# Kernel optimization log

Measured on AMD Instinct MI355X. Metric: run time of the kernel, lower is better.

Reference implementation:

```python
import jax, jax.numpy as jnp
import numpy as np

NEG_INF = float('-inf')
B, T, C, U = 32, 1000, 500, 100
RISK_FACTOR = 0.1  # risk_strategy='exp', group_strategy='end'


def _lse3(x1, x2, x3):
    # numerically-safe logsumexp of 3 args, nan-free grads at -inf
    m = jnp.maximum(jnp.maximum(x1, x2), x3)
    dead = jnp.isneginf(m)
    ms = jnp.where(dead, 0.0, m)
    s = jnp.exp(x1 - ms) + jnp.exp(x2 - ms) + jnp.exp(x3 - ms)
    s = jnp.where(dead, 1.0, s)
    return jnp.where(dead, NEG_INF, ms + jnp.log(s))


def _safe_lse(x, axis):
    m = jnp.max(x, axis=axis, keepdims=True)
    dead = jnp.isneginf(m)
    ms = jnp.where(dead, 0.0, m)
    s = jnp.sum(jnp.exp(x - ms), axis=axis, keepdims=True)
    s = jnp.where(dead, 1.0, s)
    out = jnp.where(dead, NEG_INF, ms + jnp.log(s))
    return jnp.squeeze(out, axis)


def _log_sub_exp(a, b):
    # faithful port of espnet's log_substraction_exp: log(exp(a)-exp(b))
    mask1 = (~jnp.isinf(a)) & (~jnp.isinf(b))
    a_ = jnp.where(mask1, a, -1.0)
    b_ = jnp.where(mask1, b, -2.0)
    ans_tmp = b_ + jnp.log(jnp.exp(a_ - b_) - 1.0)
    a2 = jnp.where(jnp.isinf(ans_tmp), -2000.0, a_)
    b2 = jnp.where(jnp.isinf(ans_tmp), -2001.0, b_)
    ans1 = b2 + jnp.log(jnp.exp(a2 - b2) - 1.0)
    ans = jnp.where(mask1, ans1, jnp.full_like(a, NEG_INF))
    mask2 = (~jnp.isinf(a)) & jnp.isinf(b)
    return jnp.where(mask2, a, ans)


def _shift_r(x, n):
    return jnp.pad(x[:, :-n], ((0, 0), (n, 0)), constant_values=NEG_INF)


def _shift_l(x, n):
    return jnp.pad(x[:, n:], ((0, 0), (0, n)), constant_values=NEG_INF)


def _brctc_loss(nnet_output, ys_pad, hlens, ylens):
    # Dense equivalent of the k2 CTC lattice forward-backward in the log semiring.
    Bb, Tt, Cc = nnet_output.shape
    Uu = ys_pad.shape[1]
    S = 2 * Uu + 1  # extended label states: blank,y1,blank,...,yU,blank
    dt = nnet_output.dtype
    s_idx = jnp.arange(S)
    lab = ys_pad[:, jnp.clip((s_idx - 1) // 2, 0, Uu - 1)]        # [B,S]
    labels_ext = jnp.where((s_idx % 2 == 1)[None, :], lab, 0)
    prev_lab = ys_pad[:, jnp.clip((s_idx - 3) // 2, 0, Uu - 1)]
    allow_skip = ((s_idx % 2 == 1) & (s_idx >= 3))[None, :] & (lab != prev_lab)
    # p_ext[b,t,s] = nnet_output[b,t,labels_ext[b,s]]
    p_ext = jnp.take_along_axis(
        nnet_output, jnp.broadcast_to(labels_ext[:, None, :], (Bb, Tt, S)), axis=2)
    valid_s = s_idx[None, :] <= 2 * ylens[:, None]                # states beyond 2*ylen don't exist
    p_ext = jnp.where(valid_s[:, None, :], p_ext, NEG_INF)
    p_tbs = jnp.transpose(p_ext, (1, 0, 2))                       # [T,B,S]

    # forward: alpha[t,s] includes emission at frame t
    def fstep(a, pt):
        anew = pt + _lse3(a, _shift_r(a, 1),
                          jnp.where(allow_skip, _shift_r(a, 2), NEG_INF))
        return anew, anew
    a0 = jnp.full((Bb, S), NEG_INF, dt).at[:, 0].set(0.0)  # virtual start state
    _, alpha = jax.lax.scan(fstep, a0, p_tbs)                     # [T,B,S]

    # backward: beta[t,s] covers frames t+1..hlen-1 (excludes emission at t)
    t_arr = jnp.arange(Tt)
    fin = (s_idx[None, :] == 2 * ylens[:, None]) | (s_idx[None, :] == 2 * ylens[:, None] - 1)
    beta_fin = jnp.where(fin, 0.0, NEG_INF).astype(dt)
    allow_skip_n2 = jnp.pad(allow_skip[:, 2:], ((0, 0), (0, 2)), constant_values=False)
    p_next = jnp.concatenate([p_tbs[1:], jnp.full((1, Bb, S), NEG_INF, dt)], axis=0)

    def bstep(bcarry, inp):
        t, pn = inp
        q = pn + bcarry
        cand = _lse3(q, _shift_l(q, 1),
                     jnp.where(allow_skip_n2, _shift_l(q, 2), NEG_INF))
        bnew = jnp.where((t == hlens - 1)[:, None], beta_fin, cand)
        return bnew, bnew
    _, beta = jax.lax.scan(bstep, jnp.full((Bb, S), NEG_INF, dt),
                           (t_arr, p_next), reverse=True)         # [T,B,S]

    alpha = jnp.transpose(alpha, (1, 2, 0))                       # [B,S,T]
    beta = jnp.transpose(beta, (1, 2, 0))
    alpha = jnp.where((t_arr[None, :] < hlens[:, None])[:, None, :], alpha, NEG_INF)

    # keep only label (odd) states, as in alpha[:, 1::2]
    a_l = alpha[:, 1::2, :]
    b_l = beta[:, 1::2, :]
    p_l = jnp.transpose(p_ext, (0, 2, 1))[:, 1::2, :]
    dead = jnp.isneginf(a_l)  # states absent from the lattice
    b_l = jnp.where(dead, NEG_INF, b_l)
    p_l = jnp.where(dead, NEG_INF, p_l)

    # beta' removes the self-loop continuation -> posterior of label u ending at t
    beta_prime = _log_sub_exp(b_l[:, :, :-1], b_l[:, :, 1:] + p_l[:, :, 1:])
    beta_prime = jnp.concatenate([beta_prime, b_l[:, :, -1:]], axis=-1)
    loss_state = a_l + beta_prime                                 # [B,U,T]

    # risk_strategy == 'exp': risk = -risk_factor * t / hlen
    risk = -RISK_FACTOR * (t_arr[None, None, :].astype(dt) / hlens[:, None, None].astype(dt))
    loss_state = loss_state + risk

    loss_u = _safe_lse(loss_state, 2)                             # [B,U]
    mask = ~jnp.isneginf(loss_u)
    last = jnp.sum(mask.astype(jnp.int32), axis=1) - 1            # = ylen-1
    loss = jnp.take_along_axis(loss_u, last[:, None], axis=1)[:, 0]
    return -loss


def setup_inputs():
    key = jax.random.key(0)
    k1, k2, k3, k4 = jax.random.split(key, 4)
    nnet_output = jax.nn.log_softmax(
        jax.random.normal(k1, (B, T, C), dtype=jnp.float32), axis=-1)
    ys_pad = jax.random.randint(k2, (B, U), 1, C, dtype=jnp.int32)  # labels, 0 = blank excluded
    ylens = jax.random.randint(k3, (B,), 80, U + 1, dtype=jnp.int32)
    hlens = jax.random.randint(k4, (B,), 800, T + 1, dtype=jnp.int32)
    return {'nnet_output': nnet_output, 'ys_pad': ys_pad, 'hlens': hlens, 'ylens': ylens}


def reference(nnet_output, ys_pad, hlens, ylens):
    return _brctc_loss(nnet_output, ys_pad, hlens, ylens)
```

## Files before the change

kernel.cpp:

```cpp
#include <hip/hip_runtime.h>
#include <math.h>

#define T_DIM 1000
#define C_DIM 500
#define U_DIM 100
#define PAD   16
#define AROWS (T_DIM + 5)
#define NEGINF (-INFINITY)
#define LROW  128

typedef float v2f __attribute__((ext_vector_type(2)));

__device__ __forceinline__ v2f splat2(float x) { v2f r; r[0] = x; r[1] = x; return r; }

__device__ __forceinline__ v2f lse2p(v2f X, v2f Y) {
    v2f m, mn;
    m[0]  = fmaxf(X[0], Y[0]); m[1]  = fmaxf(X[1], Y[1]);
    mn[0] = fminf(X[0], Y[0]); mn[1] = fminf(X[1], Y[1]);
    v2f d = mn - m;
    v2f e; e[0] = __expf(d[0]); e[1] = __expf(d[1]);
    v2f s = splat2(1.0f) + e;
    v2f l; l[0] = __logf(s[0]); l[1] = __logf(s[1]);
    v2f r = m + l;
    r[0] = (m[0] == NEGINF) ? NEGINF : r[0];
    r[1] = (m[1] == NEGINF) ? NEGINF : r[1];
    return r;
}

__device__ __forceinline__ v2f lse3p(v2f x1, v2f x2, v2f x3) {
    v2f m;
    m[0] = fmaxf(fmaxf(x1[0], x2[0]), x3[0]);
    m[1] = fmaxf(fmaxf(x1[1], x2[1]), x3[1]);
    v2f d1 = x1 - m, d2 = x2 - m, d3 = x3 - m;
    v2f e1, e2, e3;
    e1[0] = __expf(d1[0]); e1[1] = __expf(d1[1]);
    e2[0] = __expf(d2[0]); e2[1] = __expf(d2[1]);
    e3[0] = __expf(d3[0]); e3[1] = __expf(d3[1]);
    v2f s = (e1 + e2) + e3;
    v2f l; l[0] = __logf(s[0]); l[1] = __logf(s[1]);
    v2f r = m + l;
    r[0] = (m[0] == NEGINF) ? NEGINF : r[0];
    r[1] = (m[1] == NEGINF) ? NEGINF : r[1];
    return r;
}

__device__ __forceinline__ float lse3f(float x1, float x2, float x3) {
    float m = fmaxf(fmaxf(x1, x2), x3);
    if (m == NEGINF) return NEGINF;
    return m + __logf(__expf(x1 - m) + __expf(x2 - m) + __expf(x3 - m));
}

__device__ __forceinline__ float log_sub_expf(float a, float b) {
    bool ia = isinf(a), ib = isinf(b);
    if (!ia && !ib) {
        float ans = b + __logf(__expf(a - b) - 1.0f);
        if (isinf(ans)) ans = -2001.0f + __logf(__expf(1.0f) - 1.0f);
        return ans;
    }
    if (!ia && ib) return a;
    return NEGINF;
}

__device__ __forceinline__ float dpp_shr1(float x) {
    int r = __builtin_amdgcn_update_dpp(__float_as_int(NEGINF), __float_as_int(x),
                                        0x138, 0xF, 0xF, false);
    return __int_as_float(r);
}
__device__ __forceinline__ float dpp_shl1(float x) {
    int r = __builtin_amdgcn_update_dpp(__float_as_int(NEGINF), __float_as_int(x),
                                        0x130, 0xF, 0xF, false);
    return __int_as_float(r);
}

#define FWD_STEP(tt, PL, PBV)                                                \
    {                                                                        \
        v2f P02 = mz02 + splat2(PBV);                                        \
        float am1 = dpp_shr1(A13[1]);                                        \
        v2f Y;  Y[0] = am1;  Y[1] = A13[0];                                  \
        v2f x3; x3[0] = skip1 ? am1 : NEGINF;                                \
        x3[1] = skip3 ? A13[0] : NEGINF;                                     \
        v2f n02 = P02 + lse2p(A02, Y);                                       \
        v2f n13 = (PL) + lse3p(A13, A02, x3);                                \
        A02 = n02; A13 = n13;                                                \
        if (st)                                                              \
            ((float2*)(Ab + (size_t)(tt) * U_DIM))[L] =                      \
                make_float2(n13[0], n13[1]);                                 \
    }

#define BWD_STEP(tt, PL, PBV)                                                \
    {                                                                        \
        v2f Q02 = (mz02 + splat2(PBV)) + B02;                                \
        v2f Q13 = (PL) + B13;                                                \
        float qd0 = dpp_shl1(Q02[0]);                                        \
        float qd1 = dpp_shl1(Q13[0]);                                        \
        v2f x2; x2[0] = Q02[1]; x2[1] = qd0;                                 \
        v2f x3; x3[0] = skipA ? Q13[1] : NEGINF;                             \
        x3[1] = skipB ? qd1 : NEGINF;                                        \
        v2f n02 = lse2p(Q02, Q13);                                           \
        v2f n13 = lse3p(Q13, x2, x3);                                        \
        bool fin = ((tt) == hl - 1);                                         \
        B02[0] = fin ? f0 : n02[0]; B02[1] = fin ? f2 : n02[1];              \
        B13[0] = fin ? f1 : n13[0]; B13[1] = fin ? f3 : n13[1];              \
        if (st)                                                              \
            ((float2*)(Bb + (size_t)(tt) * U_DIM))[L] =                      \
                make_float2(B13[0], B13[1]);                                 \
    }

#define LDF(buf, rr) (((const v2f*)((buf) + (rr) * LROW))[L])

#define LSTEP(tt, RA, RB, RP)                                                \
    {                                                                        \
        float a_nx = (RA), br_nx = (RB), p_nx = (RP);                        \
        float bl   = (a_t  == NEGINF) ? NEGINF : braw_t;                     \
        float term = (a_nx == NEGINF) ? NEGINF : (br_nx + p_nx);             \
        float bp = log_sub_expf(bl, term);                                   \
        float x = a_t + bp - 0.1f * (float)(tt) * inv_hl;                    \
        if (x != NEGINF) {                                                   \
            float nm = fmaxf(m, x);                                          \
            ssum = ssum * __expf(m - nm) + __expf(x - nm);                   \
            m = nm;                                                          \
        }                                                                    \
        a_t = a_nx; braw_t = br_nx;                                          \
    }

__device__ __forceinline__ void gather_chunk(
    const float* __restrict__ nb, const int* __restrict__ shY, int yl,
    float* __restrict__ lds, float* __restrict__ ldsb,
    float* __restrict__ Pg ,
    int row0, int j)
{
#pragma unroll
    for (int k = 0; k < 15; ++k) {
        int i = j + k * 448;
        if (i < 6400) {
            int r = i >> 7, q = i & 127;
            if (q <= 100) {
                int row = row0 + r;
                int col = (q < 100) ? shY[q] : 0;
                float v = (row < T_DIM) ? nb[(size_t)row * C_DIM + col] : NEGINF;
                if (q < 100) {
                    lds[r * LROW + q] = (q < yl) ? v : NEGINF;
                    if (Pg) Pg[(size_t)r * U_DIM + q] = v;
                } else {
                    ldsb[r] = v;
                }
            }
        }
    }
}

extern "C" __global__ void __launch_bounds__(1024)
brctc_fused(const float* __restrict__ nnet, const int* __restrict__ ys,
            const int* __restrict__ hlens, const int* __restrict__ ylens,
            float* __restrict__ P,
            float* __restrict__ A, float* __restrict__ Braw,
            float* __restrict__ out)
{
    const int b = blockIdx.x;
    const int tid = threadIdx.x;
    const int w = tid >> 6, L = tid & 63;
    const int hl = hlens[b], yl = ylens[b];
    const size_t TP = T_DIM + 2 * PAD;
    const float* nb = nnet + (size_t)b * T_DIM * C_DIM;
    float* Pw = P + ((size_t)b * TP + PAD) * U_DIM;
    const float* Pb = Pw;
    const int* ysb = ys + b * U_DIM;
    float* Ab = A    + (size_t)b * AROWS * U_DIM;
    float* Bb = Braw + (size_t)b * AROWS * U_DIM;

    __shared__ __align__(16) float fbuf[2][50 * LROW];
    __shared__ __align__(16) float bbuf[2][50 * LROW];
    __shared__ float fpb[2][56], bpb[2][56];
    __shared__ float shm[8][U_DIM], shs[8][U_DIM], shlu[U_DIM];
    __shared__ int shY[U_DIM];

    if (tid < U_DIM) shY[tid] = ysb[tid];

    const int s0_ = 4 * L, s1 = 4 * L + 1, s2_ = 4 * L + 2, s3 = 4 * L + 3;
    const int u1 = 2 * L;
    const int lab1 = ysb[min(u1, U_DIM - 1)];
    const int lab3 = ysb[min(u1 + 1, U_DIM - 1)];
    const int labm = ysb[min(max(u1 - 1, 0), U_DIM - 1)];
    const int labn = ysb[min(u1 + 2, U_DIM - 1)];
    const bool skip1 = (s1 >= 3) && (lab1 != labm);
    const bool skip3 = (lab3 != lab1);
    const bool skipA = (s1 < 199) && (lab3 != lab1);
    const bool skipB = (s3 < 199) && (labn != lab3);
    const int ty = 2 * yl;
    const bool v0 = (s0_ <= 200) && (s0_ <= ty);
    const bool v2_ = (s2_ <= 200) && (s2_ <= ty);
    const bool st = (L < 50);
    v2f mz02; mz02[0] = v0 ? 0.0f : NEGINF; mz02[1] = v2_ ? 0.0f : NEGINF;
    const float f0 = (s0_ == ty || s0_ == ty - 1) ? 0.0f : NEGINF;
    const float f1 = (s1  == ty || s1  == ty - 1) ? 0.0f : NEGINF;
    const float f2 = (s2_ == ty || s2_ == ty - 1) ? 0.0f : NEGINF;
    const float f3 = (s3  == ty || s3  == ty - 1) ? 0.0f : NEGINF;

    v2f A02, A13, B02, B13;
    A02[0] = (L == 0) ? 0.0f : NEGINF; A02[1] = NEGINF;
    A13[0] = NEGINF; A13[1] = NEGINF;
    B02[0] = NEGINF; B02[1] = NEGINF;
    B13[0] = NEGINF; B13[1] = NEGINF;

    __syncthreads();

    if (w >= 2) {
        int j2 = tid - 128;
        for (int i = j2; i < 4 * 50 * 28; i += 896) {
            int buf = i / (50 * 28), rem = i % (50 * 28);
            int r = rem / 28, q = 100 + rem % 28;
            float* base = (buf == 0) ? fbuf[0] : (buf == 1) ? fbuf[1]
                        : (buf == 2) ? bbuf[0] : bbuf[1];
            base[r * LROW + q] = NEGINF;
        }
    }
    if (w >= 2 && w < 9) {
        int j = tid - 128;
        gather_chunk(nb, shY, yl, fbuf[0], fpb[0], Pw, 0, j);
        if (j < U_DIM) Pw[(size_t)T_DIM * U_DIM + j] = NEGINF;
    } else if (w >= 9) {
        int j = tid - 576;
        gather_chunk(nb, shY, yl, bbuf[0], bpb[0], nullptr, 951, j);
    }
    __syncthreads();

    for (int c = 0; c < 20; ++c) {
        if (w == 0) {
            const float* fb = fbuf[c & 1];
            const float* fp = fpb[c & 1];
            const int tb = 50 * c;
            for (int kk = 0; kk < 50; kk += 10) {
                v2f r0 = LDF(fb, kk + 0), r1 = LDF(fb, kk + 1);
                v2f r2 = LDF(fb, kk + 2), r3 = LDF(fb, kk + 3);
                v2f r4 = LDF(fb, kk + 4), r5 = LDF(fb, kk + 5);
                v2f r6 = LDF(fb, kk + 6), r7 = LDF(fb, kk + 7);
                v2f r8 = LDF(fb, kk + 8), r9 = LDF(fb, kk + 9);
                float g0 = fp[kk + 0], g1 = fp[kk + 1], g2 = fp[kk + 2];
                float g3 = fp[kk + 3], g4 = fp[kk + 4], g5 = fp[kk + 5];
                float g6 = fp[kk + 6], g7 = fp[kk + 7], g8 = fp[kk + 8];
                float g9 = fp[kk + 9];
                FWD_STEP(tb + kk + 0, r0, g0)
                FWD_STEP(tb + kk + 1, r1, g1)
                FWD_STEP(tb + kk + 2, r2, g2)
                FWD_STEP(tb + kk + 3, r3, g3)
                FWD_STEP(tb + kk + 4, r4, g4)
                FWD_STEP(tb + kk + 5, r5, g5)
                FWD_STEP(tb + kk + 6, r6, g6)
                FWD_STEP(tb + kk + 7, r7, g7)
                FWD_STEP(tb + kk + 8, r8, g8)
                FWD_STEP(tb + kk + 9, r9, g9)
            }
        } else if (w == 1) {
            const float* bbf = bbuf[c & 1];
            const float* bp  = bpb[c & 1];
            const int cc = 19 - c;
            const int tb = 50 * cc;
            for (int kk = 49; kk >= 9; kk -= 10) {
                v2f r0 = LDF(bbf, kk - 0), r1 = LDF(bbf, kk - 1);
                v2f r2 = LDF(bbf, kk - 2), r3 = LDF(bbf, kk - 3);
                v2f r4 = LDF(bbf, kk - 4), r5 = LDF(bbf, kk - 5);
                v2f r6 = LDF(bbf, kk - 6), r7 = LDF(bbf, kk - 7);
                v2f r8 = LDF(bbf, kk - 8), r9 = LDF(bbf, kk - 9);
                float g0 = bp[kk - 0], g1 = bp[kk - 1], g2 = bp[kk - 2];
                float g3 = bp[kk - 3], g4 = bp[kk - 4], g5 = bp[kk - 5];
                float g6 = bp[kk - 6], g7 = bp[kk - 7], g8 = bp[kk - 8];
                float g9 = bp[kk - 9];
                BWD_STEP(tb + kk - 0, r0, g0)
                BWD_STEP(tb + kk - 1, r1, g1)
                BWD_STEP(tb + kk - 2, r2, g2)
                BWD_STEP(tb + kk - 3, r3, g3)
                BWD_STEP(tb + kk - 4, r4, g4)
                BWD_STEP(tb + kk - 5, r5, g5)
                BWD_STEP(tb + kk - 6, r6, g6)
                BWD_STEP(tb + kk - 7, r7, g7)
                BWD_STEP(tb + kk - 8, r8, g8)
                BWD_STEP(tb + kk - 9, r9, g9)
            }
        } else if (c < 19) {
            if (w < 9) {
                int j = tid - 128;
                int row0 = (c + 1) * 50;
                gather_chunk(nb, shY, yl, fbuf[(c + 1) & 1], fpb[(c + 1) & 1],
                             Pw + (size_t)row0 * U_DIM, row0, j);
            } else {
                int j = tid - 576;
                int row0 = (18 - c) * 50 + 1;
                gather_chunk(nb, shY, yl, bbuf[(c + 1) & 1], bpb[(c + 1) & 1],
                             nullptr, row0, j);
            }
        }
        __syncthreads();
    }

    {
        const int r0f = min(hl, T_DIM);
        const int nrow = T_DIM + 1 - r0f;
        const int tot = nrow * 50;
        for (int i = tid; i < tot; i += 1024) {
            const int rr = r0f + i / 50, cc2 = i % 50;
            ((float2*)(Ab + (size_t)rr * U_DIM))[cc2] = make_float2(NEGINF, NEGINF);
        }
    }
    __syncthreads();

    {
        const int u = tid & 127;
        const int c = tid >> 7;
        if (u < U_DIM) {
            const bool valu = (u < yl);
            const float inv_hl = 1.0f / (float)hl;
            const int t0 = 125 * c;
            float a_t    = Ab[(size_t)t0 * U_DIM + u];
            float braw_t = Bb[(size_t)t0 * U_DIM + u];
            float aA0 = Ab[(long)(t0 + 1) * U_DIM + u];
            float aA1 = Ab[(long)(t0 + 2) * U_DIM + u];
            float aA2 = Ab[(long)(t0 + 3) * U_DIM + u];
            float aA3 = Ab[(long)(t0 + 4) * U_DIM + u];
            float bA0 = Bb[(long)(t0 + 1) * U_DIM + u];
            float bA1 = Bb[(long)(t0 + 2) * U_DIM + u];
            float bA2 = Bb[(long)(t0 + 3) * U_DIM + u];
            float bA3 = Bb[(long)(t0 + 4) * U_DIM + u];
            float pA0 = valu ? Pb[(long)(t0 + 1) * U_DIM + u] : NEGINF;
            float pA1 = valu ? Pb[(long)(t0 + 2) * U_DIM + u] : NEGINF;
            float pA2 = valu ? Pb[(long)(t0 + 3) * U_DIM + u] : NEGINF;
            float pA3 = valu ? Pb[(long)(t0 + 4) * U_DIM + u] : NEGINF;
            float m = NEGINF, ssum = 0.0f;
            for (int kb = 0; kb <= 120; kb += 4) {
                long nr = (long)(t0 + kb + 5);
                float aB0 = Ab[(nr + 0) * U_DIM + u];
                float aB1 = Ab[(nr + 1) * U_DIM + u];
                float aB2 = Ab[(nr + 2) * U_DIM + u];
                float aB3 = Ab[(nr + 3) * U_DIM + u];
                float bB0 = Bb[(nr + 0) * U_DIM + u];
                float bB1 = Bb[(nr + 1) * U_DIM + u];
                float bB2 = Bb[(nr + 2) * U_DIM + u];
                float bB3 = Bb[(nr + 3) * U_DIM + u];
                float pB0 = valu ? Pb[(nr + 0) * U_DIM + u] : NEGINF;
                float pB1 = valu ? Pb[(nr + 1) * U_DIM + u] : NEGINF;
                float pB2 = valu ? Pb[(nr + 2) * U_DIM + u] : NEGINF;
                float pB3 = valu ? Pb[(nr + 3) * U_DIM + u] : NEGINF;
                LSTEP(t0 + kb + 0, aA0, bA0, pA0)
                LSTEP(t0 + kb + 1, aA1, bA1, pA1)
                LSTEP(t0 + kb + 2, aA2, bA2, pA2)
                LSTEP(t0 + kb + 3, aA3, bA3, pA3)
                aA0 = aB0; aA1 = aB1; aA2 = aB2; aA3 = aB3;
                bA0 = bB0; bA1 = bB1; bA2 = bB2; bA3 = bB3;
                pA0 = pB0; pA1 = pB1; pA2 = pB2; pA3 = pB3;
            }
            LSTEP(t0 + 124, aA0, bA0, pA0)
            shm[c][u] = m; shs[c][u] = ssum;
        }
    }
    __syncthreads();
    if (tid < U_DIM) {
        float M = NEGINF;
#pragma unroll
        for (int c = 0; c < 8; ++c) M = fmaxf(M, shm[c][tid]);
        float lu = NEGINF;
        if (M != NEGINF) {
            float s = 0.0f;
#pragma unroll
            for (int c = 0; c < 8; ++c) {
                float mc = shm[c][tid];
                if (mc != NEGINF) s += shs[c][tid] * __expf(mc - M);
            }
            lu = M + __logf(s);
        }
        shlu[tid] = lu;
    }
    __syncthreads();
    if (tid == 0) {
        int cnt = 0;
        for (int u = 0; u < U_DIM; ++u) cnt += (shlu[u] != NEGINF) ? 1 : 0;
        int last = cnt - 1;
        last = last < 0 ? 0 : (last > U_DIM - 1 ? U_DIM - 1 : last);
        out[b] = -shlu[last];
    }
}

extern "C" __global__ void __launch_bounds__(256)
brctc_fwd_fb(const float* __restrict__ nnet, const int* __restrict__ ys,
             const int* __restrict__ hlens, const int* __restrict__ ylens,
             float* __restrict__ a_l)
{
    const int b = blockIdx.x;
    const int s = threadIdx.x;
    __shared__ float sh_a[201];
    __shared__ int   sh_ys[U_DIM];
    if (s < U_DIM) sh_ys[s] = ys[b * U_DIM + s];
    __syncthreads();
    const int hl = hlens[b], yl = ylens[b];
    int lab = 0; bool skip = false;
    if (s < 201) {
        if (s & 1) lab = sh_ys[(s - 1) >> 1];
        if ((s & 1) && s >= 3) skip = (sh_ys[(s - 1) >> 1] != sh_ys[(s - 3) >> 1]);
        sh_a[s] = (s == 0) ? 0.0f : NEGINF;
    }
    const bool valid = (s < 201) && (s <= 2 * yl);
    const bool isodd = (s < 201) && (s & 1);
    const int l = (s - 1) >> 1;
    const float* base = nnet + (size_t)b * T_DIM * C_DIM;
    float* alb = a_l + (size_t)b * T_DIM * U_DIM;
    __syncthreads();
    float p_cur = valid ? base[lab] : NEGINF;
    for (int t = 0; t < T_DIM; ++t) {
        float p_nxt = (valid && (t + 1 < T_DIM)) ? base[(size_t)(t + 1) * C_DIM + lab] : NEGINF;
        float x1 = (s < 201) ? sh_a[s] : NEGINF;
        float x2 = (s >= 1 && s < 201) ? sh_a[s - 1] : NEGINF;
        float x3 = skip ? sh_a[s - 2] : NEGINF;
        float anew = p_cur + lse3f(x1, x2, x3);
        __syncthreads();
        if (s < 201) sh_a[s] = anew;
        if (isodd) alb[t * U_DIM + l] = (t < hl) ? anew : NEGINF;
        __syncthreads();
        p_cur = p_nxt;
    }
}

extern "C" __global__ void __launch_bounds__(256)
brctc_bwd_fb(const float* __restrict__ nnet, const int* __restrict__ ys,
             const int* __restrict__ hlens, const int* __restrict__ ylens,
             const float* __restrict__ a_l, float* __restrict__ out)
{
    const int b = blockIdx.x;
    const int s = threadIdx.x;
    __shared__ float sh_b[201], sh_q[201], sh_lu[U_DIM];
    __shared__ int sh_ys[U_DIM];
    if (s < U_DIM) sh_ys[s] = ys[b * U_DIM + s];
    __syncthreads();
    const int hl = hlens[b], yl = ylens[b];
    int lab = 0; bool skip2 = false;
    if (s < 201) {
        if (s & 1) lab = sh_ys[(s - 1) >> 1];
        int s2 = s + 2;
        if (s2 < 201 && (s2 & 1) && s2 >= 3)
            skip2 = (sh_ys[(s2 - 1) >> 1] != sh_ys[(s2 - 3) >> 1]);
        sh_b[s] = NEGINF;
    }
    const bool valid = (s < 201) && (s <= 2 * yl);
    const bool isodd = (s < 201) && (s & 1);
    const int l = (s - 1) >> 1;
    const float fin0 = (s == 2 * yl || s == 2 * yl - 1) ? 0.0f : NEGINF;
    const float* base = nnet + (size_t)b * T_DIM * C_DIM;
    const float* alb = a_l + (size_t)b * T_DIM * U_DIM;
    float m_run = NEGINF, acc = 0.0f, prev_bl = NEGINF, p_hi = NEGINF;
    __syncthreads();
    for (int t = T_DIM - 1; t >= 0; --t) {
        float p_lo = valid ? base[(size_t)t * C_DIM + lab] : NEGINF;
        float a_cur = isodd ? alb[t * U_DIM + l] : NEGINF;
        float q = (s < 201) ? (p_hi + sh_b[s]) : NEGINF;
        if (s < 201) sh_q[s] = q;
        __syncthreads();
        float q2 = (s + 1 < 201) ? sh_q[s + 1] : NEGINF;
        float q3 = skip2 ? sh_q[s + 2] : NEGINF;
        float cand = lse3f(q, q2, q3);
        float bnew = (t == hl - 1) ? fin0 : cand;
        if (s < 201) sh_b[s] = bnew;
        if (isodd) {
            float bl_t = (a_cur == NEGINF) ? NEGINF : bnew;
            float bp = (t == T_DIM - 1) ? bl_t : log_sub_expf(bl_t, prev_bl + p_hi);
            float x = a_cur + bp - 0.1f * ((float)t / (float)hl);
            if (x != NEGINF) {
                if (x <= m_run) acc += __expf(x - m_run);
                else { acc = acc * __expf(m_run - x) + 1.0f; m_run = x; }
            }
            prev_bl = bl_t;
        }
        __syncthreads();
        p_hi = p_lo;
    }
    if (isodd) sh_lu[l] = (m_run == NEGINF) ? NEGINF : (m_run + __logf(acc));
    __syncthreads();
    if (s == 0) {
        int cnt = 0;
        for (int u = 0; u < U_DIM; ++u) cnt += (sh_lu[u] != NEGINF) ? 1 : 0;
        int last = cnt - 1;
        last = last < 0 ? 0 : (last > U_DIM - 1 ? U_DIM - 1 : last);
        out[b] = -sh_lu[last];
    }
}

extern "C" void kernel_launch(void* const* d_in, const int* in_sizes, int n_in,
                              void* d_out, int out_size, void* d_ws, size_t ws_size,
                              hipStream_t stream) {
    const float* nnet  = (const float*)d_in[0];
    const int*   ys    = (const int*)d_in[1];
    const int*   hlens = (const int*)d_in[2];
    const int*   ylens = (const int*)d_in[3];
    float*       outp  = (float*)d_out;
    const int B = in_sizes[2];
    const size_t TP = T_DIM + 2 * PAD;
    const size_t szP  = (size_t)B * TP * U_DIM;
    const size_t szA  = (size_t)B * AROWS * U_DIM;
    const size_t need = (szP + 2 * szA) * sizeof(float);

    if (ws_size >= need) {
        float* P    = (float*)d_ws;
        float* A    = P + szP;
        float* Braw = A + szA;
        brctc_fused<<<B, 1024, 0, stream>>>(nnet, ys, hlens, ylens, P, A, Braw, outp);
    } else {
        float* A = (float*)d_ws;
        brctc_fwd_fb<<<B, 256, 0, stream>>>(nnet, ys, hlens, ylens, A);
        brctc_bwd_fb<<<B, 256, 0, stream>>>(nnet, ys, hlens, ylens, A, outp);
    }
}
```

Baseline: 431.8 us.

## Split forward and backward CTC recursions across two wavefronts with LDS relay handoff

The forward and backward recursions each move from a single wavefront handling two state pairs per lane to two wavefronts, each owning half of the label range with one state per lane. Boundary values pass between the wavefronts each step through small LDS relay slots that hold a canary value, with spin-waits and periodic progress counters so the producer does not run too far ahead. The aim is to halve the serial dependency chain per wavefront. In exchange it adds spin-wait latency and LDS round trips on every step, and the gather now runs on fewer wavefronts, each with more iterations.

```diff
diff --git a/kernel.cpp b/kernel.cpp
--- a/kernel.cpp
+++ b/kernel.cpp
@@ -8,42 +8,19 @@
 #define AROWS (T_DIM + 5)
 #define NEGINF (-INFINITY)
 #define LROW  128
-
-typedef float v2f __attribute__((ext_vector_type(2)));
-
-__device__ __forceinline__ v2f splat2(float x) { v2f r; r[0] = x; r[1] = x; return r; }
-
-__device__ __forceinline__ v2f lse2p(v2f X, v2f Y) {
-    v2f m, mn;
-    m[0]  = fmaxf(X[0], Y[0]); m[1]  = fmaxf(X[1], Y[1]);
-    mn[0] = fminf(X[0], Y[0]); mn[1] = fminf(X[1], Y[1]);
-    v2f d = mn - m;
-    v2f e; e[0] = __expf(d[0]); e[1] = __expf(d[1]);
-    v2f s = splat2(1.0f) + e;
-    v2f l; l[0] = __logf(s[0]); l[1] = __logf(s[1]);
-    v2f r = m + l;
-    r[0] = (m[0] == NEGINF) ? NEGINF : r[0];
-    r[1] = (m[1] == NEGINF) ? NEGINF : r[1];
-    return r;
-}
-
-__device__ __forceinline__ v2f lse3p(v2f x1, v2f x2, v2f x3) {
-    v2f m;
-    m[0] = fmaxf(fmaxf(x1[0], x2[0]), x3[0]);
-    m[1] = fmaxf(fmaxf(x1[1], x2[1]), x3[1]);
-    v2f d1 = x1 - m, d2 = x2 - m, d3 = x3 - m;
-    v2f e1, e2, e3;
-    e1[0] = __expf(d1[0]); e1[1] = __expf(d1[1]);
-    e2[0] = __expf(d2[0]); e2[1] = __expf(d2[1]);
-    e3[0] = __expf(d3[0]); e3[1] = __expf(d3[1]);
-    v2f s = (e1 + e2) + e3;
-    v2f l; l[0] = __logf(s[0]); l[1] = __logf(s[1]);
-    v2f r = m + l;
-    r[0] = (m[0] == NEGINF) ? NEGINF : r[0];
-    r[1] = (m[1] == NEGINF) ? NEGINF : r[1];
-    return r;
-}
-
+#define CANU  0x7fbadbadu
+#define CANF  __uint_as_float(CANU)
+
+__device__ __forceinline__ float lse2s(float a, float b) {
+    float m = fmaxf(a, b), mn = fminf(a, b);
+    float r = m + __logf(1.0f + __expf(mn - m));
+    return fmaxf(r, NEGINF);
+}
+__device__ __forceinline__ float lse3s(float x1, float x2, float x3) {
+    float m = fmaxf(fmaxf(x1, x2), x3);
+    float r = m + __logf(__expf(x1 - m) + __expf(x2 - m) + __expf(x3 - m));
+    return fmaxf(r, NEGINF);
+}
 __device__ __forceinline__ float lse3f(float x1, float x2, float x3) {
     float m = fmaxf(fmaxf(x1, x2), x3);
     if (m == NEGINF) return NEGINF;
@@ -71,42 +48,6 @@
                                         0x130, 0xF, 0xF, false);
     return __int_as_float(r);
 }
-
-#define FWD_STEP(tt, PL, PBV)                                                \
-    {                                                                        \
-        v2f P02 = mz02 + splat2(PBV);                                        \
-        float am1 = dpp_shr1(A13[1]);                                        \
-        v2f Y;  Y[0] = am1;  Y[1] = A13[0];                                  \
-        v2f x3; x3[0] = skip1 ? am1 : NEGINF;                                \
-        x3[1] = skip3 ? A13[0] : NEGINF;                                     \
-        v2f n02 = P02 + lse2p(A02, Y);                                       \
-        v2f n13 = (PL) + lse3p(A13, A02, x3);                                \
-        A02 = n02; A13 = n13;                                                \
-        if (st)                                                              \
-            ((float2*)(Ab + (size_t)(tt) * U_DIM))[L] =                      \
-                make_float2(n13[0], n13[1]);                                 \
-    }
-
-#define BWD_STEP(tt, PL, PBV)                                                \
-    {                                                                        \
-        v2f Q02 = (mz02 + splat2(PBV)) + B02;                                \
-        v2f Q13 = (PL) + B13;                                                \
-        float qd0 = dpp_shl1(Q02[0]);                                        \
-        float qd1 = dpp_shl1(Q13[0]);                                        \
-        v2f x2; x2[0] = Q02[1]; x2[1] = qd0;                                 \
-        v2f x3; x3[0] = skipA ? Q13[1] : NEGINF;                             \
-        x3[1] = skipB ? qd1 : NEGINF;                                        \
-        v2f n02 = lse2p(Q02, Q13);                                           \
-        v2f n13 = lse3p(Q13, x2, x3);                                        \
-        bool fin = ((tt) == hl - 1);                                         \
-        B02[0] = fin ? f0 : n02[0]; B02[1] = fin ? f2 : n02[1];              \
-        B13[0] = fin ? f1 : n13[0]; B13[1] = fin ? f3 : n13[1];              \
-        if (st)                                                              \
-            ((float2*)(Bb + (size_t)(tt) * U_DIM))[L] =                      \
-                make_float2(B13[0], B13[1]);                                 \
-    }
-
-#define LDF(buf, rr) (((const v2f*)((buf) + (rr) * LROW))[L])
 
 #define LSTEP(tt, RA, RB, RP)                                                \
     {                                                                        \
@@ -130,8 +71,8 @@
     int row0, int j)
 {
 #pragma unroll
-    for (int k = 0; k < 15; ++k) {
-        int i = j + k * 448;
+    for (int k = 0; k < 17; ++k) {
+        int i = j + k * 384;
         if (i < 6400) {
             int r = i >> 7, q = i & 127;
             if (q <= 100) {
@@ -149,6 +90,143 @@
     }
 }
 
+#define FWP(j, pOv, gv)                                                      \
+    {                                                                        \
+        const int t_ = tbk + (j);                                            \
+        float Osh = dpp_shr1(O0);                                            \
+        float nE = (mzE_lo + (gv)) + lse2s(E0, Osh);                         \
+        float nO = (pOv) + lse3s(O0, E0, Osh + mskFlo);                      \
+        float nOsh = dpp_shr1(nO);                                           \
+        volatile float* rp = (L == 50)                                       \
+            ? (volatile float*)(rlyF + 2 * (t_ & 31)) : dmp;                 \
+        rp[0] = nOsh; rp[1] = nE;               \
+        E0 = nE; O0 = nO;                                                    \
+        if (st) stA[(j) * U_DIM] = nO;                                       \
+    }
+
+#define FWC(j, pOv, gv)                                                      \
+    {                                                                        \
+        const int t_ = tbk + (j);                                            \
+        const int sl_ = (t_ + 31) & 31;                                      \
+        float r0 = *(volatile const float*)(rlyF + 2 * sl_);                 \
+        float r1 = *(volatile const float*)(rlyF + 2 * sl_ + 1);             \
+        while (__float_as_uint(r0) == CANU || __float_as_uint(r1) == CANU) { \
+            __builtin_amdgcn_s_sleep(1);                                     \
+            r0 = *(volatile const float*)(rlyF + 2 * sl_);                   \
+            r1 = *(volatile const float*)(rlyF + 2 * sl_ + 1);               \
+        }                                                                    \
+        asm volatile("" ::: "memory");                                       \
+        float Esh = dpp_shr1(E0); Esh = (L == 0) ? r1 : Esh;                 \
+        float Osh = dpp_shr1(O0); Osh = (L == 0) ? r0 : Osh;                 \
+        float nE = (mzE_hi + (gv)) + lse2s(E0, O0);                          \
+        float nO = (pOv) + lse3s(O0, Esh, Osh + mskFhi);                     \
+        volatile float* cp = (L == 0)                                        \
+            ? (volatile float*)(rlyF + 2 * sl_) : dmp;                       \
+        cp[0] = CANF; cp[1] = CANF;                                          \
+        E0 = nE; O0 = nO;                                                    \
+        if (st) stA[(j) * U_DIM] = nO;                                       \
+        if (((t_) & 7) == 7) {                                               \
+            asm volatile("s_waitcnt lgkmcnt(0)" ::: "memory");               \
+            volatile int* pp = (L == 0) ? (volatile int*)&prgFC              \
+                                        : (volatile int*)dmp;                \
+            *pp = t_ + 1;                                                    \
+        }                                                                    \
+    }
+
+#define BWP(j, pOv, gv, FINF)                                                \
+    {                                                                        \
+        const int t_ = tbk - (j);                                            \
+        const int k_ = 999 - t_;                                             \
+        float qE = (mzE_hi + (gv)) + BE;                                     \
+        float qO = (pOv) + BO;                                               \
+        volatile float* rp = (L == 0)                                        \
+            ? (volatile float*)(rlyB + (k_ & 31)) : dmp;                     \
+        rp[0] = qO;                                                          \
+        float qOsh = dpp_shl1(qO);                                           \
+        float nE = lse2s(qE, qOsh);                                          \
+        float nO = lse3s(qO, qE, qOsh + mskBhi);                             \
+        if (FINF) { const bool fin = (t_ == hl1);                            \
+            BE = fin ? fE_hi : nE; BO = fin ? fO_hi : nO;                    \
+        } else { BE = nE; BO = nO; }                                         \
+        if (st) stB[-(int)((j) * U_DIM)] = BO;                               \
+    }
+
+#define BWC(j, pOv, gv, FINF)                                                \
+    {                                                                        \
+        const int t_ = tbk - (j);                                            \
+        const int k_ = 999 - t_;                                             \
+        const int sl_ = k_ & 31;                                             \
+        float r0 = *(volatile const float*)(rlyB + sl_);                     \
+        while (__float_as_uint(r0) == CANU) {                                \
+            __builtin_amdgcn_s_sleep(1);                                     \
+            r0 = *(volatile const float*)(rlyB + sl_);                       \
+        }                                                                    \
+        asm volatile("" ::: "memory");                                       \
+        float qE = (mzE_lo + (gv)) + BE;                                     \
+        float qO = (pOv) + BO;                                               \
+        qO = (L == 50) ? r0 : qO;                                            \
+        float qEsh = dpp_shl1(qE);                                           \
+        float qOsh = dpp_shl1(qO);                                           \
+        float nE = lse2s(qE, qO);                                            \
+        float nO = lse3s(qO, qEsh, qOsh + mskBlo);                           \
+        volatile float* cp = (L == 0)                                        \
+            ? (volatile float*)(rlyB + sl_) : dmp;                           \
+        cp[0] = CANF;                                                        \
+        if (FINF) { const bool fin = (t_ == hl1);                            \
+            BE = fin ? fE_lo : nE; BO = fin ? fO_lo : nO;                    \
+        } else { BE = nE; BO = nO; }                                         \
+        if (st) stB[-(int)((j) * U_DIM)] = BO;                               \
+        if ((k_ & 7) == 7) {                                                 \
+            asm volatile("s_waitcnt lgkmcnt(0)" ::: "memory");               \
+            volatile int* pp = (L == 0) ? (volatile int*)&prgBC              \
+                                        : (volatile int*)dmp;                \
+            *pp = k_ + 1;                                                    \
+        }                                                                    \
+    }
+
+#define BWP_BLOCK(FINF)                                                      \
+    {                                                                        \
+        const int kst = 999 - (tb2 + kk);                                    \
+        if (kst >= 30) {                                                     \
+            const int need = kst - 21;                                       \
+            while (*(volatile int*)&prgBC < need)                            \
+                __builtin_amdgcn_s_sleep(8);                                 \
+            asm volatile("" ::: "memory");                                   \
+        }                                                                    \
+        const int tbk = tb2 + kk;                                            \
+        float p0 = bb2[(kk-0)*LROW + 50 + L], p1 = bb2[(kk-1)*LROW + 50 + L],\
+              p2 = bb2[(kk-2)*LROW + 50 + L], p3 = bb2[(kk-3)*LROW + 50 + L],\
+              p4 = bb2[(kk-4)*LROW + 50 + L], p5 = bb2[(kk-5)*LROW + 50 + L],\
+              p6 = bb2[(kk-6)*LROW + 50 + L], p7 = bb2[(kk-7)*LROW + 50 + L],\
+              p8 = bb2[(kk-8)*LROW + 50 + L], p9 = bb2[(kk-9)*LROW + 50 + L];\
+        float g0 = bp2[kk-0], g1 = bp2[kk-1], g2 = bp2[kk-2], g3 = bp2[kk-3],\
+              g4 = bp2[kk-4], g5 = bp2[kk-5], g6 = bp2[kk-6], g7 = bp2[kk-7],\
+              g8 = bp2[kk-8], g9 = bp2[kk-9];                                \
+        BWP(0,p0,g0,FINF) BWP(1,p1,g1,FINF) BWP(2,p2,g2,FINF)                \
+        BWP(3,p3,g3,FINF) BWP(4,p4,g4,FINF) BWP(5,p5,g5,FINF)                \
+        BWP(6,p6,g6,FINF) BWP(7,p7,g7,FINF) BWP(8,p8,g8,FINF)                \
+        BWP(9,p9,g9,FINF)                                                    \
+        stB -= 10 * U_DIM;                                                   \
+    }
+
+#define BWC_BLOCK(FINF)                                                      \
+    {                                                                        \
+        const int tbk = tb2 + kk;                                            \
+        float p0 = bb2[(kk-0)*LROW + L], p1 = bb2[(kk-1)*LROW + L],          \
+              p2 = bb2[(kk-2)*LROW + L], p3 = bb2[(kk-3)*LROW + L],          \
+              p4 = bb2[(kk-4)*LROW + L], p5 = bb2[(kk-5)*LROW + L],          \
+              p6 = bb2[(kk-6)*LROW + L], p7 = bb2[(kk-7)*LROW + L],          \
+              p8 = bb2[(kk-8)*LROW + L], p9 = bb2[(kk-9)*LROW + L];          \
+        float g0 = bp2[kk-0], g1 = bp2[kk-1], g2 = bp2[kk-2], g3 = bp2[kk-3],\
+              g4 = bp2[kk-4], g5 = bp2[kk-5], g6 = bp2[kk-6], g7 = bp2[kk-7],\
+              g8 = bp2[kk-8], g9 = bp2[kk-9];                                \
+        BWC(0,p0,g0,FINF) BWC(1,p1,g1,FINF) BWC(2,p2,g2,FINF)                \
+        BWC(3,p3,g3,FINF) BWC(4,p4,g4,FINF) BWC(5,p5,g5,FINF)                \
+        BWC(6,p6,g6,FINF) BWC(7,p7,g7,FINF) BWC(8,p8,g8,FINF)                \
+        BWC(9,p9,g9,FINF)                                                    \
+        stB -= 10 * U_DIM;                                                   \
+    }
+
 extern "C" __global__ void __launch_bounds__(1024)
 brctc_fused(const float* __restrict__ nnet, const int* __restrict__ ys,
             const int* __restrict__ hlens, const int* __restrict__ ylens,
@@ -160,6 +238,7 @@
     const int tid = threadIdx.x;
     const int w = tid >> 6, L = tid & 63;
     const int hl = hlens[b], yl = ylens[b];
+    const int hl1 = hl - 1;
     const size_t TP = T_DIM + 2 * PAD;
     const float* nb = nnet + (size_t)b * T_DIM * C_DIM;
     float* Pw = P + ((size_t)b * TP + PAD) * U_DIM;
@@ -173,40 +252,52 @@
     __shared__ float fpb[2][56], bpb[2][56];
     __shared__ float shm[8][U_DIM], shs[8][U_DIM], shlu[U_DIM];
     __shared__ int shY[U_DIM];
+    __shared__ __align__(8) float rlyF[64];
+    __shared__ float rlyB[32];
+    __shared__ __align__(8) float dump[128];
+    __shared__ int prgFC, prgBC;
 
     if (tid < U_DIM) shY[tid] = ysb[tid];
 
-    const int s0_ = 4 * L, s1 = 4 * L + 1, s2_ = 4 * L + 2, s3 = 4 * L + 3;
-    const int u1 = 2 * L;
-    const int lab1 = ysb[min(u1, U_DIM - 1)];
-    const int lab3 = ysb[min(u1 + 1, U_DIM - 1)];
-    const int labm = ysb[min(max(u1 - 1, 0), U_DIM - 1)];
-    const int labn = ysb[min(u1 + 2, U_DIM - 1)];
-    const bool skip1 = (s1 >= 3) && (lab1 != labm);
-    const bool skip3 = (lab3 != lab1);
-    const bool skipA = (s1 < 199) && (lab3 != lab1);
-    const bool skipB = (s3 < 199) && (labn != lab3);
+    volatile float* const dmp = (volatile float*)&dump[2 * L];
+
+    const int cl = U_DIM - 1;
+    const int yL   = ysb[min(L, cl)];
+    const int yLm1 = ysb[min(max(L - 1, 0), cl)];
+    const int yLp1 = ysb[min(L + 1, cl)];
+    const int y50L = ysb[min(50 + L, cl)];
+    const int y49L = ysb[min(49 + L, cl)];
+    const int y51L = ysb[min(51 + L, cl)];
     const int ty = 2 * yl;
-    const bool v0 = (s0_ <= 200) && (s0_ <= ty);
-    const bool v2_ = (s2_ <= 200) && (s2_ <= ty);
     const bool st = (L < 50);
-    v2f mz02; mz02[0] = v0 ? 0.0f : NEGINF; mz02[1] = v2_ ? 0.0f : NEGINF;
-    const float f0 = (s0_ == ty || s0_ == ty - 1) ? 0.0f : NEGINF;
-    const float f1 = (s1  == ty || s1  == ty - 1) ? 0.0f : NEGINF;
-    const float f2 = (s2_ == ty || s2_ == ty - 1) ? 0.0f : NEGINF;
-    const float f3 = (s3  == ty || s3  == ty - 1) ? 0.0f : NEGINF;
-
-    v2f A02, A13, B02, B13;
-    A02[0] = (L == 0) ? 0.0f : NEGINF; A02[1] = NEGINF;
-    A13[0] = NEGINF; A13[1] = NEGINF;
-    B02[0] = NEGINF; B02[1] = NEGINF;
-    B13[0] = NEGINF; B13[1] = NEGINF;
-
-    __syncthreads();
-
-    if (w >= 2) {
-        int j2 = tid - 128;
-        for (int i = j2; i < 4 * 50 * 28; i += 896) {
+    const float mzE_lo = (L <= 50 && 2 * L <= ty)       ? 0.0f : NEGINF;
+    const float mzE_hi = (L <= 49 && 102 + 2 * L <= ty) ? 0.0f : NEGINF;
+    const float mskFlo = (L >= 1 && yL != yLm1)  ? 0.0f : NEGINF;
+    const float mskFhi = (y50L != y49L)          ? 0.0f : NEGINF;
+    const float mskBhi = (L <= 48 && y51L != y50L) ? 0.0f : NEGINF;
+    const float mskBlo = (yLp1 != yL)            ? 0.0f : NEGINF;
+    const float fE_lo = (2*L     == ty || 2*L     == ty-1) ? 0.0f : NEGINF;
+    const float fO_lo = (2*L+1   == ty || 2*L+1   == ty-1) ? 0.0f : NEGINF;
+    const float fE_hi = (102+2*L == ty || 102+2*L == ty-1) ? 0.0f : NEGINF;
+    const float fO_hi = (101+2*L == ty || 101+2*L == ty-1) ? 0.0f : NEGINF;
+
+    float E0, O0, BE, BO;
+    E0 = (w == 0 && L == 0) ? 0.0f : NEGINF;
+    O0 = NEGINF; BE = NEGINF; BO = NEGINF;
+
+    __syncthreads();
+
+    if (w == 0) {
+        if (L < 32) {
+            rlyF[2*L]   = (L == 31) ? NEGINF : CANF;
+            rlyF[2*L+1] = (L == 31) ? NEGINF : CANF;
+            rlyB[L] = CANF;
+        }
+        if (L == 0) { prgFC = 0; prgBC = 0; }
+    }
+    if (w >= 4) {
+        int j2 = tid - 256;
+        for (int i = j2; i < 4 * 50 * 28; i += 768) {
             int buf = i / (50 * 28), rem = i % (50 * 28);
             int r = rem / 28, q = 100 + rem % 28;
             float* base = (buf == 0) ? fbuf[0] : (buf == 1) ? fbuf[1]
@@ -214,12 +305,12 @@
             base[r * LROW + q] = NEGINF;
         }
     }
-    if (w >= 2 && w < 9) {
-        int j = tid - 128;
+    if (w >= 4 && w < 10) {
+        int j = tid - 256;
         gather_chunk(nb, shY, yl, fbuf[0], fpb[0], Pw, 0, j);
         if (j < U_DIM) Pw[(size_t)T_DIM * U_DIM + j] = NEGINF;
-    } else if (w >= 9) {
-        int j = tid - 576;
+    } else if (w >= 10) {
+        int j = tid - 640;
         gather_chunk(nb, shY, yl, bbuf[0], bpb[0], nullptr, 951, j);
     }
     __syncthreads();
@@ -229,61 +320,80 @@
             const float* fb = fbuf[c & 1];
             const float* fp = fpb[c & 1];
             const int tb = 50 * c;
+            float* stA = Ab + (size_t)tb * U_DIM + L;
             for (int kk = 0; kk < 50; kk += 10) {
-                v2f r0 = LDF(fb, kk + 0), r1 = LDF(fb, kk + 1);
-                v2f r2 = LDF(fb, kk + 2), r3 = LDF(fb, kk + 3);
-                v2f r4 = LDF(fb, kk + 4), r5 = LDF(fb, kk + 5);
-                v2f r6 = LDF(fb, kk + 6), r7 = LDF(fb, kk + 7);
-                v2f r8 = LDF(fb, kk + 8), r9 = LDF(fb, kk + 9);
-                float g0 = fp[kk + 0], g1 = fp[kk + 1], g2 = fp[kk + 2];
-                float g3 = fp[kk + 3], g4 = fp[kk + 4], g5 = fp[kk + 5];
-                float g6 = fp[kk + 6], g7 = fp[kk + 7], g8 = fp[kk + 8];
-                float g9 = fp[kk + 9];
-                FWD_STEP(tb + kk + 0, r0, g0)
-                FWD_STEP(tb + kk + 1, r1, g1)
-                FWD_STEP(tb + kk + 2, r2, g2)
-                FWD_STEP(tb + kk + 3, r3, g3)
-                FWD_STEP(tb + kk + 4, r4, g4)
-                FWD_STEP(tb + kk + 5, r5, g5)
-                FWD_STEP(tb + kk + 6, r6, g6)
-                FWD_STEP(tb + kk + 7, r7, g7)
-                FWD_STEP(tb + kk + 8, r8, g8)
-                FWD_STEP(tb + kk + 9, r9, g9)
+                if (tb + kk >= 30) {
+                    const int need = tb + kk - 21;
+                    while (*(volatile int*)&prgFC < need)
+                        __builtin_amdgcn_s_sleep(8);
+                    asm volatile("" ::: "memory");
+                }
+                const int tbk = tb + kk;
+                float p0 = fb[(kk+0)*LROW + L], p1 = fb[(kk+1)*LROW + L],
+                      p2 = fb[(kk+2)*LROW + L], p3 = fb[(kk+3)*LROW + L],
+                      p4 = fb[(kk+4)*LROW + L], p5 = fb[(kk+5)*LROW + L],
+                      p6 = fb[(kk+6)*LROW + L], p7 = fb[(kk+7)*LROW + L],
+                      p8 = fb[(kk+8)*LROW + L], p9 = fb[(kk+9)*LROW + L];
+                float g0 = fp[kk+0], g1 = fp[kk+1], g2 = fp[kk+2],
+                      g3 = fp[kk+3], g4 = fp[kk+4], g5 = fp[kk+5],
+                      g6 = fp[kk+6], g7 = fp[kk+7], g8 = fp[kk+8],
+                      g9 = fp[kk+9];
+                FWP(0,p0,g0) FWP(1,p1,g1) FWP(2,p2,g2) FWP(3,p3,g3)
+                FWP(4,p4,g4) FWP(5,p5,g5) FWP(6,p6,g6) FWP(7,p7,g7)
+                FWP(8,p8,g8) FWP(9,p9,g9)
+                stA += 10 * U_DIM;
             }
         } else if (w == 1) {
-            const float* bbf = bbuf[c & 1];
-            const float* bp  = bpb[c & 1];
+            const float* fb = fbuf[c & 1];
+            const float* fp = fpb[c & 1];
+            const int tb = 50 * c;
+            float* stA = Ab + (size_t)tb * U_DIM + 50 + L;
+            for (int kk = 0; kk < 50; kk += 10) {
+                const int tbk = tb + kk;
+                float p0 = fb[(kk+0)*LROW + 50 + L], p1 = fb[(kk+1)*LROW + 50 + L],
+                      p2 = fb[(kk+2)*LROW + 50 + L], p3 = fb[(kk+3)*LROW + 50 + L],
+                      p4 = fb[(kk+4)*LROW + 50 + L], p5 = fb[(kk+5)*LROW + 50 + L],
+                      p6 = fb[(kk+6)*LROW + 50 + L], p7 = fb[(kk+7)*LROW + 50 + L],
+                      p8 = fb[(kk+8)*LROW + 50 + L], p9 = fb[(kk+9)*LROW + 50 + L];
+                float g0 = fp[kk+0], g1 = fp[kk+1], g2 = fp[kk+2],
+                      g3 = fp[kk+3], g4 = fp[kk+4], g5 = fp[kk+5],
+                      g6 = fp[kk+6], g7 = fp[kk+7], g8 = fp[kk+8],
+                      g9 = fp[kk+9];
+                FWC(0,p0,g0) FWC(1,p1,g1) FWC(2,p2,g2) FWC(3,p3,g3)
+                FWC(4,p4,g4) FWC(5,p5,g5) FWC(6,p6,g6) FWC(7,p7,g7)
+                FWC(8,p8,g8) FWC(9,p9,g9)
+                stA += 10 * U_DIM;
+            }
+        } else if (w == 2) {
+            const float* bb2 = bbuf[c & 1];
+            const float* bp2 = bpb[c & 1];
             const int cc = 19 - c;
-            const int tb = 50 * cc;
-            for (int kk = 49; kk >= 9; kk -= 10) {
-                v2f r0 = LDF(bbf, kk - 0), r1 = LDF(bbf, kk - 1);
-                v2f r2 = LDF(bbf, kk - 2), r3 = LDF(bbf, kk - 3);
-                v2f r4 = LDF(bbf, kk - 4), r5 = LDF(bbf, kk - 5);
-                v2f r6 = LDF(bbf, kk - 6), r7 = LDF(bbf, kk - 7);
-                v2f r8 = LDF(bbf, kk - 8), r9 = LDF(bbf, kk - 9);
-                float g0 = bp[kk - 0], g1 = bp[kk - 1], g2 = bp[kk - 2];
-                float g3 = bp[kk - 3], g4 = bp[kk - 4], g5 = bp[kk - 5];
-                float g6 = bp[kk - 6], g7 = bp[kk - 7], g8 = bp[kk - 8];
-                float g9 = bp[kk - 9];
-                BWD_STEP(tb + kk - 0, r0, g0)
-                BWD_STEP(tb + kk - 1, r1, g1)
-                BWD_STEP(tb + kk - 2, r2, g2)
-                BWD_STEP(tb + kk - 3, r3, g3)
-                BWD_STEP(tb + kk - 4, r4, g4)
-                BWD_STEP(tb + kk - 5, r5, g5)
-                BWD_STEP(tb + kk - 6, r6, g6)
-                BWD_STEP(tb + kk - 7, r7, g7)
-                BWD_STEP(tb + kk - 8, r8, g8)
-                BWD_STEP(tb + kk - 9, r9, g9)
+            const int tb2 = 50 * cc;
+            float* stB = Bb + (size_t)(tb2 + 49) * U_DIM + 50 + L;
+            if (hl1 >= tb2 && hl1 <= tb2 + 49) {
+                for (int kk = 49; kk >= 9; kk -= 10) BWP_BLOCK(true)
+            } else {
+                for (int kk = 49; kk >= 9; kk -= 10) BWP_BLOCK(false)
+            }
+        } else if (w == 3) {
+            const float* bb2 = bbuf[c & 1];
+            const float* bp2 = bpb[c & 1];
+            const int cc = 19 - c;
+            const int tb2 = 50 * cc;
+            float* stB = Bb + (size_t)(tb2 + 49) * U_DIM + L;
+            if (hl1 >= tb2 && hl1 <= tb2 + 49) {
+                for (int kk = 49; kk >= 9; kk -= 10) BWC_BLOCK(true)
+            } else {
+                for (int kk = 49; kk >= 9; kk -= 10) BWC_BLOCK(false)
             }
         } else if (c < 19) {
-            if (w < 9) {
-                int j = tid - 128;
+            if (w < 10) {
+                int j = tid - 256;
                 int row0 = (c + 1) * 50;
                 gather_chunk(nb, shY, yl, fbuf[(c + 1) & 1], fpb[(c + 1) & 1],
                              Pw + (size_t)row0 * U_DIM, row0, j);
             } else {
-                int j = tid - 576;
+                int j = tid - 640;
                 int row0 = (18 - c) * 50 + 1;
                 gather_chunk(nb, shY, yl, bbuf[(c + 1) & 1], bpb[(c + 1) & 1],
                              nullptr, row0, j);
@@ -291,6 +401,9 @@
         }
         __syncthreads();
     }
+
+    if (w == 0 && st)
+        ((float2*)(Ab + (size_t)T_DIM * U_DIM))[L] = make_float2(NEGINF, NEGINF);
 
     {
         const int r0f = min(hl, T_DIM);
```

Measured after the change: 557.4 us. 1.29x slower.
